# Kernel tuning notes

Measured on AMD Instinct MI355X. Metric: run time of the kernel, lower is better.

## Reference

```python
import jax, jax.numpy as jnp
import numpy as np

H = 2            # attention heads
HID = 128        # hidden_channels
NEG_SLOPE = 0.2  # GATConv leaky_relu slope

N_USER, N_POST, N_ENT = 100000, 50000, 20000
TEXT_D, USER_D, ENT_D = 768, 64, 64
E_PUB, E_REP, E_CON, E_INT, E_FOL = 150000, 300000, 200000, 500000, 500000


def _gat(h_src, h_dst, src, dst, Wsrc, Wdst, asrc, adst, bias):
    """PyG GATConv((-1,-1), C, heads=H, concat=False, add_self_loops=False)."""
    n_dst = h_dst.shape[0]
    C = Wsrc.shape[1] // H
    xs = (h_src @ Wsrc).reshape(-1, H, C)          # [Ns,H,C]
    xd = (h_dst @ Wdst).reshape(-1, H, C)          # [Nd,H,C]
    al_s = jnp.einsum('nhc,hc->nh', xs, asrc)      # [Ns,H]
    al_d = jnp.einsum('nhc,hc->nh', xd, adst)      # [Nd,H]
    e = jax.nn.leaky_relu(al_s[src] + al_d[dst], NEG_SLOPE)   # [E,H]
    m = jax.ops.segment_max(e, dst, num_segments=n_dst)
    m = jnp.where(jnp.isfinite(m), m, 0.0)
    ex = jnp.exp(e - m[dst])
    denom = jax.ops.segment_sum(ex, dst, num_segments=n_dst)
    alpha = ex / (denom[dst] + 1e-16)              # per-dst softmax
    msg = xs[src] * alpha[:, :, None]              # [E,H,C]
    out = jax.ops.segment_sum(msg, dst, num_segments=n_dst)   # [Nd,H,C]
    return out.mean(axis=1) + bias                 # concat=False -> head mean


def setup_inputs() -> dict:
    key = jax.random.key(0)
    ks = jax.random.split(key, 24)
    s = 0.05
    d = {
        'post_cls': jax.random.normal(ks[0], (N_POST, TEXT_D), jnp.float32),
        'user_x': jax.random.normal(ks[1], (N_USER, USER_D), jnp.float32),
        'entity_x': jax.random.normal(ks[2], (N_ENT, ENT_D), jnp.float32),
        'Wpost': jax.random.normal(ks[3], (TEXT_D, HID), jnp.float32) * s,
        'bpost': jnp.zeros((HID,), jnp.float32),
        'Wuser': jax.random.normal(ks[4], (USER_D, HID), jnp.float32) * s,
        'buser': jnp.zeros((HID,), jnp.float32),
        'Went': jax.random.normal(ks[5], (ENT_D, HID), jnp.float32) * s,
        'bent': jnp.zeros((HID,), jnp.float32),
        # 2 layers x 5 relations (publish, repost, contain, interact, follow)
        'gat_Wsrc': jax.random.normal(ks[6], (2, 5, HID, H * HID), jnp.float32) * s,
        'gat_Wdst': jax.random.normal(ks[7], (2, 5, HID, H * HID), jnp.float32) * s,
        'gat_asrc': jax.random.normal(ks[8], (2, 5, H, HID), jnp.float32) * s,
        'gat_adst': jax.random.normal(ks[9], (2, 5, H, HID), jnp.float32) * s,
        'gat_bias': jnp.zeros((2, 5, HID), jnp.float32),
        'Wc1': jax.random.normal(ks[10], (HID, HID // 2), jnp.float32) * s,
        'bc1': jnp.zeros((HID // 2,), jnp.float32),
        'Wc2': jax.random.normal(ks[11], (HID // 2, 1), jnp.float32) * s,
        'bc2': jnp.zeros((1,), jnp.float32),
        'pub_src': jax.random.randint(ks[12], (E_PUB,), 0, N_USER, jnp.int32),
        'pub_dst': jax.random.randint(ks[13], (E_PUB,), 0, N_POST, jnp.int32),
        'rep_src': jax.random.randint(ks[14], (E_REP,), 0, N_USER, jnp.int32),
        'rep_dst': jax.random.randint(ks[15], (E_REP,), 0, N_POST, jnp.int32),
        'con_src': jax.random.randint(ks[16], (E_CON,), 0, N_POST, jnp.int32),
        'con_dst': jax.random.randint(ks[17], (E_CON,), 0, N_ENT, jnp.int32),
        'int_src': jax.random.randint(ks[18], (E_INT,), 0, N_USER, jnp.int32),
        'int_dst': jax.random.randint(ks[19], (E_INT,), 0, N_USER, jnp.int32),
        'fol_src': jax.random.randint(ks[20], (E_FOL,), 0, N_USER, jnp.int32),
        'fol_dst': jax.random.randint(ks[21], (E_FOL,), 0, N_USER, jnp.int32),
    }
    return d


def _forward(post_cls, user_x, entity_x, Wpost, bpost, Wuser, buser, Went, bent,
             gat_Wsrc, gat_Wdst, gat_asrc, gat_adst, gat_bias,
             Wc1, bc1, Wc2, bc2, edges):
    h = {
        'post': post_cls @ Wpost + bpost,
        'user': user_x @ Wuser + buser,
        'entity': entity_x @ Went + bent,
    }
    for l in range(2):
        def g(r, h_src, h_dst, src, dst):
            return _gat(h_src, h_dst, src, dst,
                        gat_Wsrc[l, r], gat_Wdst[l, r],
                        gat_asrc[l, r], gat_adst[l, r], gat_bias[l, r])
        # HeteroConv aggr='sum' over edge types sharing a dst node type
        new_post = (g(0, h['user'], h['post'], edges['pub_src'], edges['pub_dst'])
                    + g(1, h['user'], h['post'], edges['rep_src'], edges['rep_dst']))
        new_ent = g(2, h['post'], h['entity'], edges['con_src'], edges['con_dst'])
        new_user = (g(3, h['user'], h['user'], edges['int_src'], edges['int_dst'])
                    + g(4, h['user'], h['user'], edges['fol_src'], edges['fol_dst']))
        h = {'post': jax.nn.relu(new_post),
             'user': jax.nn.relu(new_user),
             'entity': jax.nn.relu(new_ent)}
    # classifier (dropout inactive at inference)
    z = jax.nn.relu(h['post'] @ Wc1 + bc1)
    out = z @ Wc2 + bc2
    return out.squeeze(-1)   # [n_posts]


def reference(post_cls, user_x, entity_x, Wpost, bpost, Wuser, buser, Went, bent,
              gat_Wsrc, gat_Wdst, gat_asrc, gat_adst, gat_bias,
              Wc1, bc1, Wc2, bc2,
              pub_src, pub_dst, rep_src, rep_dst, con_src, con_dst,
              int_src, int_dst, fol_src, fol_dst):
    edges = dict(pub_src=pub_src, pub_dst=pub_dst, rep_src=rep_src, rep_dst=rep_dst,
                 con_src=con_src, con_dst=con_dst, int_src=int_src, int_dst=int_dst,
                 fol_src=fol_src, fol_dst=fol_dst)
    return _forward(post_cls, user_x, entity_x, Wpost, bpost, Wuser, buser, Went, bent,
                    gat_Wsrc, gat_Wdst, gat_asrc, gat_adst, gat_bias,
                    Wc1, bc1, Wc2, bc2, edges)
```

## Files before the change

kernel.cpp:

```cpp
#include <hip/hip_runtime.h>
#include <cstdint>
#include <cstddef>

#define N_USER 100000
#define N_POST 50000
#define TEXT_D 768
#define USER_D 64
#define E_PUB 150000
#define E_REP 300000
#define E_INT 500000
#define E_FOL 500000
#define E_TOT 1450000
#define N_TOT 300000

typedef unsigned short ushort_t;
typedef float f4v __attribute__((ext_vector_type(4)));
typedef short s8v __attribute__((ext_vector_type(8)));
typedef unsigned short u4v __attribute__((ext_vector_type(4)));

__device__ __forceinline__ float leaky(float v) { return v > 0.f ? v : 0.2f * v; }
__device__ __forceinline__ void split_bf(float x, ushort_t& hi, ushort_t& lo) {
  unsigned u = __float_as_uint(x);
  hi = (ushort_t)(u >> 16);
  float r = x - __uint_as_float(u & 0xFFFF0000u);
  lo = (ushort_t)(__float_as_uint(r) >> 16);
}

struct Ptrs4 { const int* p[4]; };

__global__ void wvec_kernel(const float* __restrict__ W, const float* __restrict__ av,
                            float* __restrict__ wv) {
  int b = blockIdx.x;
  int lr = b / 2, h = b % 2;
  const float* Wp = W + ((size_t)lr * 128 * 256) + (size_t)threadIdx.x * 256 + h * 128;
  const float* ap = av + (size_t)(lr * 2 + h) * 128;
  float acc = 0.f;
  for (int c = 0; c < 128; ++c) acc += Wp[c] * ap[c];
  wv[(size_t)(lr * 2 + h) * 128 + threadIdx.x] = acc;
}

__global__ void wt_prep(const float* __restrict__ W, ushort_t* __restrict__ WTh,
                        ushort_t* __restrict__ WTl, int K, int C) {
  int k = blockIdx.x * 256 + threadIdx.x;
  int c = blockIdx.y;
  if (k >= K) return;
  ushort_t h, l;
  split_bf(W[(size_t)k * C + c], h, l);
  WTh[(size_t)c * K + k] = h;
  WTl[(size_t)c * K + k] = l;
}

__global__ void stk_prep(const float* __restrict__ Wa, const float* __restrict__ Wb,
                         ushort_t* __restrict__ STh, ushort_t* __restrict__ STl) {
  int rel = blockIdx.x;
  int c = blockIdx.y;
  int t = threadIdx.x;
  const float* W = rel ? Wb : Wa;
  float v = W[(size_t)(t & 127) * 256 + (size_t)(t >> 7) * 128 + c];
  ushort_t hh, ll;
  split_bf(v, hh, ll);
  size_t idx = (size_t)c * 512 + (size_t)rel * 256 + t;
  STh[idx] = hh;
  STl[idx] = ll;
}

__global__ void bias_sum(const float* __restrict__ gbias, float* __restrict__ BS) {
  int c = threadIdx.x;
  BS[c]       = gbias[0 * 640 + 0 * 128 + c] + gbias[0 * 640 + 1 * 128 + c];
  BS[128 + c] = gbias[0 * 640 + 3 * 128 + c] + gbias[0 * 640 + 4 * 128 + c];
  BS[256 + c] = gbias[1 * 640 + 0 * 128 + c] + gbias[1 * 640 + 1 * 128 + c];
}

template <int CF, bool BIAS, bool RELU>
__global__ __launch_bounds__(256) void gemm_mfma(const float* __restrict__ X,
                                                 const ushort_t* __restrict__ WTh,
                                                 const ushort_t* __restrict__ WTl,
                                                 const float* __restrict__ bv,
                                                 float* __restrict__ Out,
                                                 int N, int K) {
  __shared__ ushort_t Ah[64][32], Al[64][32];
  __shared__ ushort_t Bh[CF * 16][32], Bl[CF * 16][32];
  int t = threadIdx.x;
  int L = t & 63;
  int wv = t >> 6;
  int m = L & 15, quad = L >> 4;
  int row0 = blockIdx.x * 64;

  f4v acc[CF];
#pragma unroll
  for (int cf = 0; cf < CF; ++cf) acc[cf] = (f4v){0.f, 0.f, 0.f, 0.f};

  int nk = K >> 5;
  for (int kb = 0; kb < nk; ++kb) {
    int k0 = kb * 32;
#pragma unroll
    for (int i = 0; i < 2; ++i) {
      int s = t + 256 * i;
      int r = s >> 3, k4 = s & 7;
      int row = row0 + r;
      float4 v = make_float4(0.f, 0.f, 0.f, 0.f);
      if (row < N) v = *(const float4*)(X + (size_t)row * K + k0 + k4 * 4);
      ushort_t hx, lx, hy, ly, hz, lz, hw, lw;
      split_bf(v.x, hx, lx); split_bf(v.y, hy, ly);
      split_bf(v.z, hz, lz); split_bf(v.w, hw, lw);
      u4v h, l;
      h[0] = hx; h[1] = hy; h[2] = hz; h[3] = hw;
      l[0] = lx; l[1] = ly; l[2] = lz; l[3] = lw;
      *(u4v*)&Ah[r][k4 * 4] = h;
      *(u4v*)&Al[r][k4 * 4] = l;
    }
#pragma unroll
    for (int i = 0; i < CF / 4; ++i) {
      int s = t + 256 * i;
      int c = s >> 2, ch = s & 3;
      *(s8v*)&Bh[c][ch * 8] = *(const s8v*)(WTh + (size_t)c * K + k0 + ch * 8);
      *(s8v*)&Bl[c][ch * 8] = *(const s8v*)(WTl + (size_t)c * K + k0 + ch * 8);
    }
    __syncthreads();
    s8v a_h = *(const s8v*)&Ah[wv * 16 + m][quad * 8];
    s8v a_l = *(const s8v*)&Al[wv * 16 + m][quad * 8];
#pragma unroll
    for (int cf = 0; cf < CF; ++cf) {
      s8v b_h = *(const s8v*)&Bh[cf * 16 + m][quad * 8];
      s8v b_l = *(const s8v*)&Bl[cf * 16 + m][quad * 8];
      acc[cf] = __builtin_amdgcn_mfma_f32_16x16x32_bf16(a_h, b_h, acc[cf], 0, 0, 0);
      acc[cf] = __builtin_amdgcn_mfma_f32_16x16x32_bf16(a_h, b_l, acc[cf], 0, 0, 0);
      acc[cf] = __builtin_amdgcn_mfma_f32_16x16x32_bf16(a_l, b_h, acc[cf], 0, 0, 0);
    }
    __syncthreads();
  }

  float bvs[CF];
#pragma unroll
  for (int cf = 0; cf < CF; ++cf) bvs[cf] = BIAS ? bv[cf * 16 + m] : 0.f;
#pragma unroll
  for (int j = 0; j < 4; ++j) {
    int row = row0 + wv * 16 + quad * 4 + j;
    if (row < N) {
      float* o = Out + (size_t)row * (CF * 16) + m;
#pragma unroll
      for (int cf = 0; cf < CF; ++cf) {
        float vv = acc[cf][j] + bvs[cf];
        if (RELU) vv = fmaxf(vv, 0.f);
        o[cf * 16] = vv;
      }
    }
  }
}

__device__ __forceinline__ void rel_of(int g, int& r, int& loc, int& nb) {
  if (g < 450000) {
    if (g < 150000) { r = 0; loc = g;          nb = 0; }
    else            { r = 1; loc = g - 150000; nb = 50000; }
  } else if (g < 950000)  { r = 2; loc = g - 450000;  nb = 100000; }
  else                    { r = 3; loc = g - 950000;  nb = 200000; }
}
__global__ void histc_kernel(Ptrs4 dsts, int* __restrict__ cnt) {
  int g = blockIdx.x * 256 + threadIdx.x;
  if (g >= E_TOT) return;
  int r, loc, nb;
  rel_of(g, r, loc, nb);
  atomicAdd(&cnt[nb + dsts.p[r][loc]], 1);
}
__global__ __launch_bounds__(256) void scan1_kernel(const int* __restrict__ cnt,
                                                    int* __restrict__ excl,
                                                    int* __restrict__ partials, int Nd) {
  __shared__ int sb[256];
  int t = threadIdx.x;
  int base = blockIdx.x * 1024 + t * 4;
  int v[4];
#pragma unroll
  for (int j = 0; j < 4; ++j) v[j] = (base + j < Nd) ? cnt[base + j] : 0;
  int tot = v[0] + v[1] + v[2] + v[3];
  sb[t] = tot;
  __syncthreads();
  for (int off = 1; off < 256; off <<= 1) {
    int x = 0;
    if (t >= off) x = sb[t - off];
    __syncthreads();
    sb[t] += x;
    __syncthreads();
  }
  int ex = sb[t] - tot;
  if (t == 255) partials[blockIdx.x] = sb[t];
  int run = ex;
#pragma unroll
  for (int j = 0; j < 4; ++j) {
    if (base + j < Nd) excl[base + j] = run;
    run += v[j];
  }
}
__global__ __launch_bounds__(512) void scan2_kernel(int* __restrict__ partials, int B) {
  __shared__ int sb[512];
  int t = threadIdx.x;
  int v = (t < B) ? partials[t] : 0;
  sb[t] = v;
  __syncthreads();
  for (int off = 1; off < 512; off <<= 1) {
    int x = 0;
    if (t >= off) x = sb[t - off];
    __syncthreads();
    sb[t] += x;
    __syncthreads();
  }
  if (t < B) partials[t] = sb[t] - v;
}
__global__ void scan3_kernel(const int* __restrict__ excl, const int* __restrict__ partials,
                             int* __restrict__ rowptr, int* __restrict__ cursor) {
  int i = blockIdx.x * 256 + threadIdx.x;
  if (i < N_TOT) {
    int v = excl[i] + partials[i >> 10];
    rowptr[i] = v;
    cursor[i] = v;
  }
  if (i == 0) rowptr[N_TOT] = E_TOT;
}
__global__ void scatterc_kernel(Ptrs4 srcs, Ptrs4 dsts,
                                int* __restrict__ cursor, int* __restrict__ csrc) {
  int g = blockIdx.x * 256 + threadIdx.x;
  if (g >= E_TOT) return;
  int r, loc, nb;
  rel_of(g, r, loc, nb);
  int p = atomicAdd(&cursor[nb + dsts.p[r][loc]], 1);
  csrc[p] = srcs.p[r][loc];
}

__global__ __launch_bounds__(256) void logits2_kernel(const float* __restrict__ H,
                                                      const float* __restrict__ wsA,
                                                      const float* __restrict__ wsB,
                                                      float* __restrict__ alsA,
                                                      float* __restrict__ alsB, int Ns) {
  int n = blockIdx.x * 4 + (threadIdx.x >> 6);
  int lane = threadIdx.x & 63;
  if (n >= Ns) return;
  const float* hr = H + (size_t)n * 128;
  float ha = hr[lane], hb = hr[lane + 64];
  float p0 = ha * wsA[lane] + hb * wsA[lane + 64];
  float p1 = ha * wsA[128 + lane] + hb * wsA[192 + lane];
  float p2 = ha * wsB[lane] + hb * wsB[lane + 64];
  float p3 = ha * wsB[128 + lane] + hb * wsB[192 + lane];
#pragma unroll
  for (int mk = 32; mk; mk >>= 1) {
    p0 += __shfl_xor(p0, mk); p1 += __shfl_xor(p1, mk);
    p2 += __shfl_xor(p2, mk); p3 += __shfl_xor(p3, mk);
  }
  if (lane == 0) {
    *(float2*)(alsA + 2 * (size_t)n) = make_float2(p0, p1);
    *(float2*)(alsB + 2 * (size_t)n) = make_float2(p2, p3);
  }
}

__device__ __forceinline__ void dst_tvals(const float* __restrict__ Hd, const float* __restrict__ wdv,
                                          int d, int lane, float& t0, float& t1) {
  const float* hr = Hd + (size_t)d * 128;
  float ha = hr[lane], hb = hr[lane + 64];
  t0 = ha * wdv[lane] + hb * wdv[lane + 64];
  t1 = ha * wdv[128 + lane] + hb * wdv[192 + lane];
#pragma unroll
  for (int mk = 32; mk; mk >>= 1) { t0 += __shfl_xor(t0, mk); t1 += __shfl_xor(t1, mk); }
}

__device__ __forceinline__ void aggG_rel(const int* __restrict__ rowptr,
                                         const int* __restrict__ csrc,
                                         const float* __restrict__ als,
                                         const float* __restrict__ Hs,
                                         float t0, float t1, int d, int h, int s,
                                         int lane, float* __restrict__ Grow) {
  int start = rowptr[d], end = rowptr[d + 1];
  float den0 = 0.f, den1 = 0.f;
  float a0[4] = {0.f, 0.f, 0.f, 0.f}, a1[4] = {0.f, 0.f, 0.f, 0.f};
  if (end > start) {
    int last = end - 1;
    for (int b0 = start; b0 < end; b0 += 4) {
      int eA = b0 + h, eB = b0 + 2 + h;
      bool vA = eA < end, vB = eB < end;
      eA = vA ? eA : last;
      eB = vB ? eB : last;
      int sA = csrc[eA], sB = csrc[eB];
      float2 alA = *(const float2*)(als + 2 * (size_t)sA);
      float2 alB = *(const float2*)(als + 2 * (size_t)sB);
      f4v xA = *(const f4v*)(Hs + (size_t)sA * 128 + 4 * s);
      f4v xB = *(const f4v*)(Hs + (size_t)sB * 128 + 4 * s);
      float wA0 = vA ? __expf(leaky(alA.x + t0)) : 0.f;
      float wA1 = vA ? __expf(leaky(alA.y + t1)) : 0.f;
      float wB0 = vB ? __expf(leaky(alB.x + t0)) : 0.f;
      float wB1 = vB ? __expf(leaky(alB.y + t1)) : 0.f;
      den0 += wA0 + wB0;
      den1 += wA1 + wB1;
#pragma unroll
      for (int j = 0; j < 4; ++j) {
        a0[j] += wA0 * xA[j] + wB0 * xB[j];
        a1[j] += wA1 * xA[j] + wB1 * xB[j];
      }
    }
  }
  den0 += __shfl_xor(den0, 32);
  den1 += __shfl_xor(den1, 32);
  float i0 = 0.5f / (den0 + 1e-16f);
  float i1 = 0.5f / (den1 + 1e-16f);
  f4v o0, o1;
#pragma unroll
  for (int j = 0; j < 4; ++j) {
    float u = a0[j] + __shfl_xor(a0[j], 32);
    float v = a1[j] + __shfl_xor(a1[j], 32);
    o0[j] = u * i0;
    o1[j] = v * i1;
  }
  if (lane < 32) {
    *(f4v*)(Grow + 4 * s) = o0;
    *(f4v*)(Grow + 128 + 4 * s) = o1;
  }
}

__global__ __launch_bounds__(256) void aggG2_kernel(const int* __restrict__ rowA,
                                                    const int* __restrict__ rowB,
                                                    const int* __restrict__ csrc,
                                                    const float* __restrict__ alsA,
                                                    const float* __restrict__ alsB,
                                                    const float* __restrict__ wdvA,
                                                    const float* __restrict__ wdvB,
                                                    const float* __restrict__ Hs,
                                                    const float* __restrict__ Hd,
                                                    float* __restrict__ G,
                                                    int Nd, int dOff) {
  int dl = blockIdx.x * 4 + (threadIdx.x >> 6);
  int lane = threadIdx.x & 63;
  if (dl >= Nd) return;
  int d = dl + dOff;
  float tA0, tA1, tB0, tB1;
  dst_tvals(Hd, wdvA, d, lane, tA0, tA1);
  dst_tvals(Hd, wdvB, d, lane, tB0, tB1);
  int h = lane >> 5, s = lane & 31;
  float* Grow = G + (size_t)dl * 512;
  aggG_rel(rowA, csrc, alsA, Hs, tA0, tA1, d, h, s, lane, Grow);
  aggG_rel(rowB, csrc, alsB, Hs, tB0, tB1, d, h, s, lane, Grow + 256);
}

__global__ __launch_bounds__(256) void classifier_kernel(const float* __restrict__ Hp,
                                                         const float* __restrict__ Wc1, const float* __restrict__ bc1,
                                                         const float* __restrict__ Wc2, const float* __restrict__ bc2,
                                                         float* __restrict__ out, int N) {
  __shared__ float sW[128 * 64];
  int t = threadIdx.x;
#pragma unroll
  for (int i = 0; i < 8; ++i) ((float4*)sW)[t + 256 * i] = ((const float4*)Wc1)[t + 256 * i];
  __syncthreads();
  int lane = t & 63, wv = t >> 6;
  float b = bc1[lane], w2 = Wc2[lane], b2 = bc2[0];
#pragma unroll
  for (int nn = 0; nn < 2; ++nn) {
    int n = blockIdx.x * 8 + wv * 2 + nn;
    if (n >= N) continue;
    const float* hr = Hp + (size_t)n * 128;
    float accz = b;
    for (int k = 0; k < 128; ++k) accz += hr[k] * sW[k * 64 + lane];
    float z = fmaxf(accz, 0.f) * w2;
#pragma unroll
    for (int off = 32; off; off >>= 1) z += __shfl_down(z, off);
    if (lane == 0) out[n] = z + b2;
  }
}

extern "C" void kernel_launch(void* const* d_in, const int* in_sizes, int n_in,
                              void* d_out, int out_size, void* d_ws, size_t ws_size,
                              hipStream_t stream) {
  const float* post_cls = (const float*)d_in[0];
  const float* user_x   = (const float*)d_in[1];
  const float* Wpost = (const float*)d_in[3];
  const float* bpost = (const float*)d_in[4];
  const float* Wuser = (const float*)d_in[5];
  const float* buser = (const float*)d_in[6];
  const float* gWsrc = (const float*)d_in[9];
  const float* gWdst = (const float*)d_in[10];
  const float* gasrc = (const float*)d_in[11];
  const float* gadst = (const float*)d_in[12];
  const float* gbias = (const float*)d_in[13];
  const float* Wc1 = (const float*)d_in[14];
  const float* bc1 = (const float*)d_in[15];
  const float* Wc2 = (const float*)d_in[16];
  const float* bc2 = (const float*)d_in[17];
  Ptrs4 SRCS, DSTS;
  SRCS.p[0] = (const int*)d_in[18]; DSTS.p[0] = (const int*)d_in[19];
  SRCS.p[1] = (const int*)d_in[20]; DSTS.p[1] = (const int*)d_in[21];
  SRCS.p[2] = (const int*)d_in[24]; DSTS.p[2] = (const int*)d_in[25];
  SRCS.p[3] = (const int*)d_in[26]; DSTS.p[3] = (const int*)d_in[27];
  float* out = (float*)d_out;
  (void)ws_size; (void)in_sizes; (void)n_in; (void)out_size;

  float* Wf = (float*)d_ws;
  size_t o = 0;
  float* WDSTV = Wf + o; o += 2560;
  float* WSRCV = Wf + o; o += 2560;
  float* BS    = Wf + o; o += 384;
  float* ALSa  = Wf + o; o += (size_t)N_USER * 2;
  float* ALSb  = Wf + o; o += (size_t)N_USER * 2;
  float* HU    = Wf + o; o += (size_t)N_USER * 128;
  float* HP    = Wf + o; o += (size_t)N_POST * 128;
  float* G     = Wf + o; o += (size_t)N_POST * 512;
  float* TMP   = Wf + o; o += (size_t)N_POST * 128;
  int* Wi = (int*)(Wf + o);
  size_t io = 0;
  int* RP   = Wi + io; io += N_TOT + 1;
  int* CURS = Wi + io; io += N_TOT;
  int* CNT  = Wi + io; io += N_TOT;
  int* EXCL = Wi + io; io += N_TOT;
  int* PART = Wi + io; io += 512;
  int* CSRC = Wi + io; io += E_TOT;
  io = (io + 7) & ~(size_t)7;
  ushort_t* Wu = (ushort_t*)(Wi + io);
  size_t uo = 0;
  ushort_t* PWh = Wu + uo; uo += 128 * TEXT_D;
  ushort_t* PWl = Wu + uo; uo += 128 * TEXT_D;
  ushort_t* UWh = Wu + uo; uo += 128 * USER_D;
  ushort_t* UWl = Wu + uo; uo += 128 * USER_D;
  ushort_t* STh[3]; ushort_t* STl[3];
  for (int i = 0; i < 3; ++i) {
    STh[i] = Wu + uo; uo += 128 * 512;
    STl[i] = Wu + uo; uo += 128 * 512;
  }

  const int NOFF_PUB = 0, NOFF_REP = 50000, NOFF_INT = 100000, NOFF_FOL = 200000;

  (void)hipMemsetAsync(CNT, 0, (size_t)N_TOT * sizeof(int), stream);
  histc_kernel<<<(E_TOT + 255) / 256, 256, 0, stream>>>(DSTS, CNT);
  int B = (N_TOT + 1023) / 1024;
  scan1_kernel<<<B, 256, 0, stream>>>(CNT, EXCL, PART, N_TOT);
  scan2_kernel<<<1, 512, 0, stream>>>(PART, B);
  scan3_kernel<<<(N_TOT + 255) / 256, 256, 0, stream>>>(EXCL, PART, RP, CURS);
  scatterc_kernel<<<(E_TOT + 255) / 256, 256, 0, stream>>>(SRCS, DSTS, CURS, CSRC);

  wt_prep<<<dim3(3, 128), 256, 0, stream>>>(Wpost, PWh, PWl, TEXT_D, 128);
  wt_prep<<<dim3(1, 128), 256, 0, stream>>>(Wuser, UWh, UWl, USER_D, 128);
  stk_prep<<<dim3(2, 128), 256, 0, stream>>>(gWsrc + (size_t)0 * 32768, gWsrc + (size_t)1 * 32768, STh[0], STl[0]);
  stk_prep<<<dim3(2, 128), 256, 0, stream>>>(gWsrc + (size_t)3 * 32768, gWsrc + (size_t)4 * 32768, STh[1], STl[1]);
  stk_prep<<<dim3(2, 128), 256, 0, stream>>>(gWsrc + (size_t)5 * 32768, gWsrc + (size_t)6 * 32768, STh[2], STl[2]);
  wvec_kernel<<<20, 128, 0, stream>>>(gWdst, gadst, WDSTV);
  wvec_kernel<<<20, 128, 0, stream>>>(gWsrc, gasrc, WSRCV);
  bias_sum<<<1, 128, 0, stream>>>(gbias, BS);

  gemm_mfma<8, true, false><<<(N_POST + 63) / 64, 256, 0, stream>>>(
      post_cls, PWh, PWl, bpost, HP, N_POST, TEXT_D);
  gemm_mfma<8, true, false><<<(N_USER + 63) / 64, 256, 0, stream>>>(
      user_x, UWh, UWl, buser, HU, N_USER, USER_D);

  logits2_kernel<<<(N_USER + 3) / 4, 256, 0, stream>>>(
      HU, WSRCV + 0 * 256, WSRCV + 1 * 256, ALSa, ALSb, N_USER);
  aggG2_kernel<<<(N_POST + 3) / 4, 256, 0, stream>>>(
      RP + NOFF_PUB, RP + NOFF_REP, CSRC, ALSa, ALSb,
      WDSTV + 0 * 256, WDSTV + 1 * 256, HU, HP, G, N_POST, 0);
  gemm_mfma<8, true, true><<<(N_POST + 63) / 64, 256, 0, stream>>>(
      G, STh[0], STl[0], BS + 0, HP, N_POST, 512);

  logits2_kernel<<<(N_USER + 3) / 4, 256, 0, stream>>>(
      HU, WSRCV + 3 * 256, WSRCV + 4 * 256, ALSa, ALSb, N_USER);
  aggG2_kernel<<<(50000 + 3) / 4, 256, 0, stream>>>(
      RP + NOFF_INT, RP + NOFF_FOL, CSRC, ALSa, ALSb,
      WDSTV + 3 * 256, WDSTV + 4 * 256, HU, HU, G, 50000, 0);
  gemm_mfma<8, true, true><<<(50000 + 63) / 64, 256, 0, stream>>>(
      G, STh[1], STl[1], BS + 128, TMP, 50000, 512);
  aggG2_kernel<<<(50000 + 3) / 4, 256, 0, stream>>>(
      RP + NOFF_INT, RP + NOFF_FOL, CSRC, ALSa, ALSb,
      WDSTV + 3 * 256, WDSTV + 4 * 256, HU, HU, G, 50000, 50000);
  gemm_mfma<8, true, true><<<(50000 + 63) / 64, 256, 0, stream>>>(
      G, STh[1], STl[1], BS + 128, HU + (size_t)50000 * 128, 50000, 512);
  (void)hipMemcpyAsync(HU, TMP, (size_t)50000 * 128 * sizeof(float),
                       hipMemcpyDeviceToDevice, stream);

  logits2_kernel<<<(N_USER + 3) / 4, 256, 0, stream>>>(
      HU, WSRCV + 5 * 256, WSRCV + 6 * 256, ALSa, ALSb, N_USER);
  aggG2_kernel<<<(N_POST + 3) / 4, 256, 0, stream>>>(
      RP + NOFF_PUB, RP + NOFF_REP, CSRC, ALSa, ALSb,
      WDSTV + 5 * 256, WDSTV + 6 * 256, HU, HP, G, N_POST, 0);
  gemm_mfma<8, true, true><<<(N_POST + 63) / 64, 256, 0, stream>>>(
      G, STh[2], STl[2], BS + 256, HP, N_POST, 512);

  classifier_kernel<<<(N_POST + 7) / 8, 256, 0, stream>>>(HP, Wc1, bc1, Wc2, bc2, out, N_POST);
}
```

Measured before the change: 1.096 ms.

## Pipeline MFMA GEMM with double-buffered LDS and pre-split bf16 aggregation output

Replaces the single-buffered GEMM with a double-buffered version that issues global loads for the next K tile into registers while the MFMAs for the current tile run. It also uses a 2x2 wave tiling with padded LDS rows to cut bank conflicts and reuse A/B fragments. The aggregation kernel now gives each relation its own half-wave, gathers 8 edges per step for more memory-level parallelism, and writes its output already split into hi/lo bf16. This removes the fp32 G buffer and the per-tile split inside the GEMM. In exchange it uses more registers and LDS, which may lower occupancy.

```diff
diff --git a/kernel.cpp b/kernel.cpp
--- a/kernel.cpp
+++ b/kernel.cpp
@@ -6,10 +6,6 @@
 #define N_POST 50000
 #define TEXT_D 768
 #define USER_D 64
-#define E_PUB 150000
-#define E_REP 300000
-#define E_INT 500000
-#define E_FOL 500000
 #define E_TOT 1450000
 #define N_TOT 300000
 
@@ -17,6 +13,7 @@
 typedef float f4v __attribute__((ext_vector_type(4)));
 typedef short s8v __attribute__((ext_vector_type(8)));
 typedef unsigned short u4v __attribute__((ext_vector_type(4)));
+typedef unsigned short u8v __attribute__((ext_vector_type(8)));
 
 __device__ __forceinline__ float leaky(float v) { return v > 0.f ? v : 0.2f * v; }
 __device__ __forceinline__ void split_bf(float x, ushort_t& hi, ushort_t& lo) {
@@ -71,81 +68,169 @@
   BS[256 + c] = gbias[1 * 640 + 0 * 128 + c] + gbias[1 * 640 + 1 * 128 + c];
 }
 
-template <int CF, bool BIAS, bool RELU>
-__global__ __launch_bounds__(256) void gemm_mfma(const float* __restrict__ X,
-                                                 const ushort_t* __restrict__ WTh,
-                                                 const ushort_t* __restrict__ WTl,
+template <bool ASPLIT, bool RELU>
+__global__ __launch_bounds__(256) void gemm_pipe(const void* __restrict__ Ag,
+                                                 const ushort_t* __restrict__ Agl,
+                                                 const ushort_t* __restrict__ Bgh,
+                                                 const ushort_t* __restrict__ Bgl,
                                                  const float* __restrict__ bv,
                                                  float* __restrict__ Out,
                                                  int N, int K) {
-  __shared__ ushort_t Ah[64][32], Al[64][32];
-  __shared__ ushort_t Bh[CF * 16][32], Bl[CF * 16][32];
+  __shared__ ushort_t LAh[2][64 * 40], LAl[2][64 * 40];
+  __shared__ ushort_t LBh[2][128 * 40], LBl[2][128 * 40];
   int t = threadIdx.x;
-  int L = t & 63;
-  int wv = t >> 6;
-  int m = L & 15, quad = L >> 4;
+  int lane = t & 63, w = t >> 6;
+  int m = lane & 15, quad = lane >> 4;
+  int wr = w >> 1, wc = w & 1;
   int row0 = blockIdx.x * 64;
-
-  f4v acc[CF];
-#pragma unroll
-  for (int cf = 0; cf < CF; ++cf) acc[cf] = (f4v){0.f, 0.f, 0.f, 0.f};
-
-  int nk = K >> 5;
-  for (int kb = 0; kb < nk; ++kb) {
-    int k0 = kb * 32;
+  int nkb = K >> 5;
+
+  const float* Xf = (const float*)Ag;
+  const ushort_t* Xh = (const ushort_t*)Ag;
+
+  int arf[2], af4[2];
+  int ars = 0, ags = 0;
+  if (!ASPLIT) {
 #pragma unroll
     for (int i = 0; i < 2; ++i) {
-      int s = t + 256 * i;
-      int r = s >> 3, k4 = s & 7;
+      int p = t + 256 * i;
+      int r = p >> 3;
       int row = row0 + r;
-      float4 v = make_float4(0.f, 0.f, 0.f, 0.f);
-      if (row < N) v = *(const float4*)(X + (size_t)row * K + k0 + k4 * 4);
-      ushort_t hx, lx, hy, ly, hz, lz, hw, lw;
-      split_bf(v.x, hx, lx); split_bf(v.y, hy, ly);
-      split_bf(v.z, hz, lz); split_bf(v.w, hw, lw);
-      u4v h, l;
-      h[0] = hx; h[1] = hy; h[2] = hz; h[3] = hw;
-      l[0] = lx; l[1] = ly; l[2] = lz; l[3] = lw;
-      *(u4v*)&Ah[r][k4 * 4] = h;
-      *(u4v*)&Al[r][k4 * 4] = l;
+      arf[i] = (row < N) ? row : (N - 1);
+      af4[i] = p & 7;
     }
-#pragma unroll
-    for (int i = 0; i < CF / 4; ++i) {
-      int s = t + 256 * i;
-      int c = s >> 2, ch = s & 3;
-      *(s8v*)&Bh[c][ch * 8] = *(const s8v*)(WTh + (size_t)c * K + k0 + ch * 8);
-      *(s8v*)&Bl[c][ch * 8] = *(const s8v*)(WTl + (size_t)c * K + k0 + ch * 8);
+  } else {
+    int r = t >> 2;
+    int row = row0 + r;
+    ars = (row < N) ? row : (N - 1);
+    ags = t & 3;
+  }
+  int bc_[2], bg_[2];
+#pragma unroll
+  for (int i = 0; i < 2; ++i) {
+    int p = t + 256 * i;
+    bc_[i] = p >> 2;
+    bg_[i] = p & 3;
+  }
+
+  f4v acc[2][4];
+#pragma unroll
+  for (int mt = 0; mt < 2; ++mt)
+#pragma unroll
+    for (int ct = 0; ct < 4; ++ct) acc[mt][ct] = (f4v){0.f, 0.f, 0.f, 0.f};
+
+  float4 pa0[2], pa1[2];
+  u8v pah0, pal0, pah1, pal1;
+  u8v pbh0[2], pbl0[2], pbh1[2], pbl1[2];
+
+#define LOADG(S, KB)                                                          \
+  do {                                                                        \
+    int k0 = (KB) * 32;                                                       \
+    if (ASPLIT) {                                                             \
+      pah##S = *(const u8v*)(Xh + (size_t)ars * K + k0 + ags * 8);            \
+      pal##S = *(const u8v*)(Agl + (size_t)ars * K + k0 + ags * 8);           \
+    } else {                                                                  \
+      _Pragma("unroll")                                                       \
+      for (int i = 0; i < 2; ++i)                                             \
+        pa##S[i] = *(const float4*)(Xf + (size_t)arf[i] * K + k0 + af4[i] * 4);\
+    }                                                                         \
+    _Pragma("unroll")                                                         \
+    for (int i = 0; i < 2; ++i) {                                             \
+      pbh##S[i] = *(const u8v*)(Bgh + (size_t)bc_[i] * K + k0 + bg_[i] * 8);  \
+      pbl##S[i] = *(const u8v*)(Bgl + (size_t)bc_[i] * K + k0 + bg_[i] * 8);  \
+    }                                                                         \
+  } while (0)
+
+#define WRITES(S)                                                             \
+  do {                                                                        \
+    if (ASPLIT) {                                                             \
+      int r = t >> 2, g = t & 3;                                              \
+      *(u8v*)&LAh[S][r * 40 + g * 8] = pah##S;                                \
+      *(u8v*)&LAl[S][r * 40 + g * 8] = pal##S;                                \
+    } else {                                                                  \
+      _Pragma("unroll")                                                       \
+      for (int i = 0; i < 2; ++i) {                                           \
+        int p = t + 256 * i;                                                  \
+        int r = p >> 3, f4i = p & 7;                                          \
+        u4v hh, ll;                                                           \
+        ushort_t sh, sl;                                                      \
+        split_bf(pa##S[i].x, sh, sl); hh[0] = sh; ll[0] = sl;                 \
+        split_bf(pa##S[i].y, sh, sl); hh[1] = sh; ll[1] = sl;                 \
+        split_bf(pa##S[i].z, sh, sl); hh[2] = sh; ll[2] = sl;                 \
+        split_bf(pa##S[i].w, sh, sl); hh[3] = sh; ll[3] = sl;                 \
+        *(u4v*)&LAh[S][r * 40 + f4i * 4] = hh;                                \
+        *(u4v*)&LAl[S][r * 40 + f4i * 4] = ll;                                \
+      }                                                                       \
+    }                                                                         \
+    _Pragma("unroll")                                                         \
+    for (int i = 0; i < 2; ++i) {                                             \
+      int c = bc_[i], g = bg_[i];                                             \
+      *(u8v*)&LBh[S][c * 40 + g * 8] = pbh##S[i];                             \
+      *(u8v*)&LBl[S][c * 40 + g * 8] = pbl##S[i];                             \
+    }                                                                         \
+  } while (0)
+
+  auto MF = [&](int buf) {
+    s8v ah[2], al2[2];
+#pragma unroll
+    for (int mt = 0; mt < 2; ++mt) {
+      int r = wr * 32 + mt * 16 + m;
+      ah[mt] = *(const s8v*)&LAh[buf][r * 40 + quad * 8];
+      al2[mt] = *(const s8v*)&LAl[buf][r * 40 + quad * 8];
     }
-    __syncthreads();
-    s8v a_h = *(const s8v*)&Ah[wv * 16 + m][quad * 8];
-    s8v a_l = *(const s8v*)&Al[wv * 16 + m][quad * 8];
-#pragma unroll
-    for (int cf = 0; cf < CF; ++cf) {
-      s8v b_h = *(const s8v*)&Bh[cf * 16 + m][quad * 8];
-      s8v b_l = *(const s8v*)&Bl[cf * 16 + m][quad * 8];
-      acc[cf] = __builtin_amdgcn_mfma_f32_16x16x32_bf16(a_h, b_h, acc[cf], 0, 0, 0);
-      acc[cf] = __builtin_amdgcn_mfma_f32_16x16x32_bf16(a_h, b_l, acc[cf], 0, 0, 0);
-      acc[cf] = __builtin_amdgcn_mfma_f32_16x16x32_bf16(a_l, b_h, acc[cf], 0, 0, 0);
-    }
-    __syncthreads();
-  }
-
-  float bvs[CF];
-#pragma unroll
-  for (int cf = 0; cf < CF; ++cf) bvs[cf] = BIAS ? bv[cf * 16 + m] : 0.f;
-#pragma unroll
-  for (int j = 0; j < 4; ++j) {
-    int row = row0 + wv * 16 + quad * 4 + j;
-    if (row < N) {
-      float* o = Out + (size_t)row * (CF * 16) + m;
-#pragma unroll
-      for (int cf = 0; cf < CF; ++cf) {
-        float vv = acc[cf][j] + bvs[cf];
-        if (RELU) vv = fmaxf(vv, 0.f);
-        o[cf * 16] = vv;
+#pragma unroll
+    for (int ct = 0; ct < 4; ++ct) {
+      int c = wc * 64 + ct * 16 + m;
+      s8v bh = *(const s8v*)&LBh[buf][c * 40 + quad * 8];
+      s8v bl = *(const s8v*)&LBl[buf][c * 40 + quad * 8];
+#pragma unroll
+      for (int mt = 0; mt < 2; ++mt) {
+        acc[mt][ct] = __builtin_amdgcn_mfma_f32_16x16x32_bf16(ah[mt], bh, acc[mt][ct], 0, 0, 0);
+        acc[mt][ct] = __builtin_amdgcn_mfma_f32_16x16x32_bf16(ah[mt], bl, acc[mt][ct], 0, 0, 0);
+        acc[mt][ct] = __builtin_amdgcn_mfma_f32_16x16x32_bf16(al2[mt], bh, acc[mt][ct], 0, 0, 0);
       }
     }
-  }
+  };
+
+  LOADG(0, 0);
+  if (nkb > 1) LOADG(1, 1);
+  int kb = 0;
+  for (; kb + 2 <= nkb; kb += 2) {
+    WRITES(0);
+    __syncthreads();
+    if (kb + 2 < nkb) LOADG(0, kb + 2);
+    MF(0);
+    WRITES(1);
+    __syncthreads();
+    if (kb + 3 < nkb) LOADG(1, kb + 3);
+    MF(1);
+  }
+  if (kb < nkb) {
+    WRITES(0);
+    __syncthreads();
+    MF(0);
+  }
+#undef LOADG
+#undef WRITES
+
+  float bb[4];
+#pragma unroll
+  for (int ct = 0; ct < 4; ++ct) bb[ct] = bv[wc * 64 + ct * 16 + m];
+#pragma unroll
+  for (int mt = 0; mt < 2; ++mt)
+#pragma unroll
+    for (int j = 0; j < 4; ++j) {
+      int row = row0 + wr * 32 + mt * 16 + quad * 4 + j;
+      if (row < N) {
+        float* o = Out + (size_t)row * 128 + wc * 64 + m;
+#pragma unroll
+        for (int ct = 0; ct < 4; ++ct) {
+          float vv = acc[mt][ct][j] + bb[ct];
+          if (RELU) vv = fmaxf(vv, 0.f);
+          o[ct * 16] = vv;
+        }
+      }
+    }
 }
 
 __device__ __forceinline__ void rel_of(int g, int& r, int& loc, int& nb) {
@@ -250,68 +335,6 @@
   }
 }
 
-__device__ __forceinline__ void dst_tvals(const float* __restrict__ Hd, const float* __restrict__ wdv,
-                                          int d, int lane, float& t0, float& t1) {
-  const float* hr = Hd + (size_t)d * 128;
-  float ha = hr[lane], hb = hr[lane + 64];
-  t0 = ha * wdv[lane] + hb * wdv[lane + 64];
-  t1 = ha * wdv[128 + lane] + hb * wdv[192 + lane];
-#pragma unroll
-  for (int mk = 32; mk; mk >>= 1) { t0 += __shfl_xor(t0, mk); t1 += __shfl_xor(t1, mk); }
-}
-
-__device__ __forceinline__ void aggG_rel(const int* __restrict__ rowptr,
-                                         const int* __restrict__ csrc,
-                                         const float* __restrict__ als,
-                                         const float* __restrict__ Hs,
-                                         float t0, float t1, int d, int h, int s,
-                                         int lane, float* __restrict__ Grow) {
-  int start = rowptr[d], end = rowptr[d + 1];
-  float den0 = 0.f, den1 = 0.f;
-  float a0[4] = {0.f, 0.f, 0.f, 0.f}, a1[4] = {0.f, 0.f, 0.f, 0.f};
-  if (end > start) {
-    int last = end - 1;
-    for (int b0 = start; b0 < end; b0 += 4) {
-      int eA = b0 + h, eB = b0 + 2 + h;
-      bool vA = eA < end, vB = eB < end;
-      eA = vA ? eA : last;
-      eB = vB ? eB : last;
-      int sA = csrc[eA], sB = csrc[eB];
-      float2 alA = *(const float2*)(als + 2 * (size_t)sA);
-      float2 alB = *(const float2*)(als + 2 * (size_t)sB);
-      f4v xA = *(const f4v*)(Hs + (size_t)sA * 128 + 4 * s);
-      f4v xB = *(const f4v*)(Hs + (size_t)sB * 128 + 4 * s);
-      float wA0 = vA ? __expf(leaky(alA.x + t0)) : 0.f;
-      float wA1 = vA ? __expf(leaky(alA.y + t1)) : 0.f;
-      float wB0 = vB ? __expf(leaky(alB.x + t0)) : 0.f;
-      float wB1 = vB ? __expf(leaky(alB.y + t1)) : 0.f;
-      den0 += wA0 + wB0;
-      den1 += wA1 + wB1;
-#pragma unroll
-      for (int j = 0; j < 4; ++j) {
-        a0[j] += wA0 * xA[j] + wB0 * xB[j];
-        a1[j] += wA1 * xA[j] + wB1 * xB[j];
-      }
-    }
-  }
-  den0 += __shfl_xor(den0, 32);
-  den1 += __shfl_xor(den1, 32);
-  float i0 = 0.5f / (den0 + 1e-16f);
-  float i1 = 0.5f / (den1 + 1e-16f);
-  f4v o0, o1;
-#pragma unroll
-  for (int j = 0; j < 4; ++j) {
-    float u = a0[j] + __shfl_xor(a0[j], 32);
-    float v = a1[j] + __shfl_xor(a1[j], 32);
-    o0[j] = u * i0;
-    o1[j] = v * i1;
-  }
-  if (lane < 32) {
-    *(f4v*)(Grow + 4 * s) = o0;
-    *(f4v*)(Grow + 128 + 4 * s) = o1;
-  }
-}
-
 __global__ __launch_bounds__(256) void aggG2_kernel(const int* __restrict__ rowA,
                                                     const int* __restrict__ rowB,
                                                     const int* __restrict__ csrc,
@@ -321,19 +344,75 @@
                                                     const float* __restrict__ wdvB,
                                                     const float* __restrict__ Hs,
                                                     const float* __restrict__ Hd,
-                                                    float* __restrict__ G,
+                                                    ushort_t* __restrict__ Gh,
+                                                    ushort_t* __restrict__ Gl,
                                                     int Nd, int dOff) {
-  int dl = blockIdx.x * 4 + (threadIdx.x >> 6);
+  int w = threadIdx.x >> 6;
   int lane = threadIdx.x & 63;
+  int rel = w & 1;
+  int hw = lane >> 5, s = lane & 31;
+  int dl = blockIdx.x * 4 + (w >> 1) * 2 + hw;
   if (dl >= Nd) return;
   int d = dl + dOff;
-  float tA0, tA1, tB0, tB1;
-  dst_tvals(Hd, wdvA, d, lane, tA0, tA1);
-  dst_tvals(Hd, wdvB, d, lane, tB0, tB1);
-  int h = lane >> 5, s = lane & 31;
-  float* Grow = G + (size_t)dl * 512;
-  aggG_rel(rowA, csrc, alsA, Hs, tA0, tA1, d, h, s, lane, Grow);
-  aggG_rel(rowB, csrc, alsB, Hs, tB0, tB1, d, h, s, lane, Grow + 256);
+  const int* rp = rel ? rowB : rowA;
+  const float* als = rel ? alsB : alsA;
+  const float* wdv = rel ? wdvB : wdvA;
+
+  const float* hr = Hd + (size_t)d * 128;
+  float t0 = 0.f, t1 = 0.f;
+#pragma unroll
+  for (int j = 0; j < 4; ++j) {
+    float hv = hr[s + 32 * j];
+    t0 += hv * wdv[s + 32 * j];
+    t1 += hv * wdv[128 + s + 32 * j];
+  }
+#pragma unroll
+  for (int mk = 16; mk; mk >>= 1) { t0 += __shfl_xor(t0, mk); t1 += __shfl_xor(t1, mk); }
+
+  int start = rp[d], end = rp[d + 1];
+  float den0 = 0.f, den1 = 0.f;
+  f4v a0 = (f4v){0.f, 0.f, 0.f, 0.f}, a1 = (f4v){0.f, 0.f, 0.f, 0.f};
+  if (end > start) {
+    int last = end - 1;
+    for (int b0 = start; b0 < end; b0 += 8) {
+      int sid[8]; bool vl[8];
+#pragma unroll
+      for (int j = 0; j < 8; ++j) {
+        int ee = b0 + j;
+        vl[j] = ee < end;
+        sid[j] = csrc[vl[j] ? ee : last];
+      }
+      float2 al[8]; f4v x[8];
+#pragma unroll
+      for (int j = 0; j < 8; ++j) {
+        al[j] = *(const float2*)(als + 2 * (size_t)sid[j]);
+        x[j] = *(const f4v*)(Hs + (size_t)sid[j] * 128 + 4 * s);
+      }
+#pragma unroll
+      for (int j = 0; j < 8; ++j) {
+        float w0 = vl[j] ? __expf(leaky(al[j].x + t0)) : 0.f;
+        float w1 = vl[j] ? __expf(leaky(al[j].y + t1)) : 0.f;
+        den0 += w0; den1 += w1;
+#pragma unroll
+        for (int q = 0; q < 4; ++q) { a0[q] += w0 * x[j][q]; a1[q] += w1 * x[j][q]; }
+      }
+    }
+  }
+  float i0 = 0.5f / (den0 + 1e-16f);
+  float i1 = 0.5f / (den1 + 1e-16f);
+  ushort_t* gh = Gh + (size_t)dl * 512 + rel * 256;
+  ushort_t* gl = Gl + (size_t)dl * 512 + rel * 256;
+  u4v g0h, g0l, g1h, g1l;
+#pragma unroll
+  for (int q = 0; q < 4; ++q) {
+    ushort_t hh, ll;
+    split_bf(a0[q] * i0, hh, ll); g0h[q] = hh; g0l[q] = ll;
+    split_bf(a1[q] * i1, hh, ll); g1h[q] = hh; g1l[q] = ll;
+  }
+  *(u4v*)(gh + 4 * s) = g0h;
+  *(u4v*)(gl + 4 * s) = g0l;
+  *(u4v*)(gh + 128 + 4 * s) = g1h;
+  *(u4v*)(gl + 128 + 4 * s) = g1l;
 }
 
 __global__ __launch_bounds__(256) void classifier_kernel(const float* __restrict__ Hp,
@@ -396,7 +475,6 @@
   float* ALSb  = Wf + o; o += (size_t)N_USER * 2;
   float* HU    = Wf + o; o += (size_t)N_USER * 128;
   float* HP    = Wf + o; o += (size_t)N_POST * 128;
-  float* G     = Wf + o; o += (size_t)N_POST * 512;
   float* TMP   = Wf + o; o += (size_t)N_POST * 128;
   int* Wi = (int*)(Wf + o);
   size_t io = 0;
@@ -418,6 +496,8 @@
     STh[i] = Wu + uo; uo += 128 * 512;
     STl[i] = Wu + uo; uo += 128 * 512;
   }
+  ushort_t* Gh = Wu + uo; uo += (size_t)N_POST * 512;
+  ushort_t* Gl = Wu + uo; uo += (size_t)N_POST * 512;
 
   const int NOFF_PUB = 0, NOFF_REP = 50000, NOFF_INT = 100000, NOFF_FOL = 200000;
 
@@ -438,31 +518,31 @@
   wvec_kernel<<<20, 128, 0, stream>>>(gWsrc, gasrc, WSRCV);
   bias_sum<<<1, 128, 0, stream>>>(gbias, BS);
 
-  gemm_mfma<8, true, false><<<(N_POST + 63) / 64, 256, 0, stream>>>(
-      post_cls, PWh, PWl, bpost, HP, N_POST, TEXT_D);
-  gemm_mfma<8, true, false><<<(N_USER + 63) / 64, 256, 0, stream>>>(
-      user_x, UWh, UWl, buser, HU, N_USER, USER_D);
+  gemm_pipe<false, false><<<(N_POST + 63) / 64, 256, 0, stream>>>(
+      post_cls, nullptr, PWh, PWl, bpost, HP, N_POST, TEXT_D);
+  gemm_pipe<false, false><<<(N_USER + 63) / 64, 256, 0, stream>>>(
+      user_x, nullptr, UWh, UWl, buser, HU, N_USER, USER_D);
 
   logits2_kernel<<<(N_USER + 3) / 4, 256, 0, stream>>>(
       HU, WSRCV + 0 * 256, WSRCV + 1 * 256, ALSa, ALSb, N_USER);
   aggG2_kernel<<<(N_POST + 3) / 4, 256, 0, stream>>>(
       RP + NOFF_PUB, RP + NOFF_REP, CSRC, ALSa, ALSb,
-      WDSTV + 0 * 256, WDSTV + 1 * 256, HU, HP, G, N_POST, 0);
-  gemm_mfma<8, true, true><<<(N_POST + 63) / 64, 256, 0, stream>>>(
-      G, STh[0], STl[0], BS + 0, HP, N_POST, 512);
+      WDSTV + 0 * 256, WDSTV + 1 * 256, HU, HP, Gh, Gl, N_POST, 0);
+  gemm_pipe<true, true><<<(N_POST + 63) / 64, 256, 0, stream>>>(
+      Gh, Gl, STh[0], STl[0], BS + 0, HP, N_POST, 512);
 
   logits2_kernel<<<(N_USER + 3) / 4, 256, 0, stream>>>(
       HU, WSRCV + 3 * 256, WSRCV + 4 * 256, ALSa, ALSb, N_USER);
   aggG2_kernel<<<(50000 + 3) / 4, 256, 0, stream>>>(
       RP + NOFF_INT, RP + NOFF_FOL, CSRC, ALSa, ALSb,
-      WDSTV + 3 * 256, WDSTV + 4 * 256, HU, HU, G, 50000, 0);
-  gemm_mfma<8, true, true><<<(50000 + 63) / 64, 256, 0, stream>>>(
-      G, STh[1], STl[1], BS + 128, TMP, 50000, 512);
+      WDSTV + 3 * 256, WDSTV + 4 * 256, HU, HU, Gh, Gl, 50000, 0);
+  gemm_pipe<true, true><<<(50000 + 63) / 64, 256, 0, stream>>>(
+      Gh, Gl, STh[1], STl[1], BS + 128, TMP, 50000, 512);
   aggG2_kernel<<<(50000 + 3) / 4, 256, 0, stream>>>(
       RP + NOFF_INT, RP + NOFF_FOL, CSRC, ALSa, ALSb,
-      WDSTV + 3 * 256, WDSTV + 4 * 256, HU, HU, G, 50000, 50000);
-  gemm_mfma<8, true, true><<<(50000 + 63) / 64, 256, 0, stream>>>(
-      G, STh[1], STl[1], BS + 128, HU + (size_t)50000 * 128, 50000, 512);
+      WDSTV + 3 * 256, WDSTV + 4 * 256, HU, HU, Gh, Gl, 50000, 50000);
+  gemm_pipe<true, true><<<(50000 + 63) / 64, 256, 0, stream>>>(
+      Gh, Gl, STh[1], STl[1], BS + 128, HU + (size_t)50000 * 128, 50000, 512);
   (void)hipMemcpyAsync(HU, TMP, (size_t)50000 * 128 * sizeof(float),
                        hipMemcpyDeviceToDevice, stream);
 
@@ -470,9 +550,9 @@
       HU, WSRCV + 5 * 256, WSRCV + 6 * 256, ALSa, ALSb, N_USER);
   aggG2_kernel<<<(N_POST + 3) / 4, 256, 0, stream>>>(
       RP + NOFF_PUB, RP + NOFF_REP, CSRC, ALSa, ALSb,
-      WDSTV + 5 * 256, WDSTV + 6 * 256, HU, HP, G, N_POST, 0);
-  gemm_mfma<8, true, true><<<(N_POST + 63) / 64, 256, 0, stream>>>(
-      G, STh[2], STl[2], BS + 256, HP, N_POST, 512);
+      WDSTV + 5 * 256, WDSTV + 6 * 256, HU, HP, Gh, Gl, N_POST, 0);
+  gemm_pipe<true, true><<<(N_POST + 63) / 64, 256, 0, stream>>>(
+      Gh, Gl, STh[2], STl[2], BS + 256, HP, N_POST, 512);
 
   classifier_kernel<<<(N_POST + 7) / 8, 256, 0, stream>>>(HP, Wc1, bc1, Wc2, bc2, out, N_POST);
 }
```

Measured after the change: 1.125 ms. 1.03x slower.
